# Performance work log

Measured on AMD Instinct MI355X. Metric: run time of the kernel, lower is better.

## Reference

```python
import jax, jax.numpy as jnp
import numpy as np

E = 2048   # embedding_size
H = 16     # n_heads
D = E // H # head_dimension = 128
B = 4
N = 2048


def setup_inputs() -> dict:
    key = jax.random.key(0)
    ks = jax.random.split(key, 5)
    scale_qkv = 1.0 / np.sqrt(E)
    scale_fc = 1.0 / np.sqrt(E)
    return {
        "x": jax.random.normal(ks[0], (B, N, E), dtype=jnp.float32),
        # torch Linear(E, E + 2*D); stored as [in, out] for x @ W
        "w_qkv": jax.random.uniform(ks[1], (E, E + 2 * D), jnp.float32, -scale_qkv, scale_qkv),
        "b_qkv": jax.random.uniform(ks[2], (E + 2 * D,), jnp.float32, -scale_qkv, scale_qkv),
        "w_fc": jax.random.uniform(ks[3], (E, E), jnp.float32, -scale_fc, scale_fc),
        "b_fc": jax.random.uniform(ks[4], (E,), jnp.float32, -scale_fc, scale_fc),
    }


def reference(x, w_qkv, b_qkv, w_fc, b_fc):
    b, n, _ = x.shape
    qkv = x @ w_qkv + b_qkv                         # [B,N,E+2D]
    q = qkv[..., :E].reshape(b, n, H, D)            # [B,N,H,D]
    k = qkv[..., E:E + D]                           # [B,N,D] single KV head (MQA)
    v = qkv[..., E + D:]                            # [B,N,D]
    # scores: queries per head against shared keys
    scores = jnp.einsum("bnhd,bmd->bhnm", q, k) / jnp.sqrt(jnp.float32(D))
    # causal mask: triu(ones, diagonal=1) positions filled with -inf
    causal = jnp.triu(jnp.ones((n, n), dtype=bool), k=1)
    scores = jnp.where(causal, -jnp.inf, scores)
    attn = jax.nn.softmax(scores, axis=-1)          # [B,H,N,N]
    out = jnp.einsum("bhnm,bmd->bnhd", attn, v)     # [B,N,H,D]
    out = out.reshape(b, n, E)
    return out @ w_fc + b_fc                        # dropout=0 (eval): identity
```

## Files before the change

kernel.cpp:

```cpp
#include <hip/hip_runtime.h>

#define E_DIM 2048
#define H_NUM 16
#define D_HEAD 128
#define B_SZ 4
#define N_SEQ 2048
#define QKV_LD 2304
#define MROWS_T (B_SZ * N_SEQ)
#define PLS 40
#define SC2F 0.12751744802582937f

typedef __attribute__((ext_vector_type(8))) __bf16 bfx8;
typedef __attribute__((ext_vector_type(8))) short sx8;
typedef __attribute__((ext_vector_type(4))) short sx4;
typedef __attribute__((ext_vector_type(4))) float fx4;

__device__ __forceinline__ fx4 mfma_bf16(bfx8 a, bfx8 b, fx4 c) {
    return __builtin_amdgcn_mfma_f32_16x16x32_bf16(a, b, c, 0, 0, 0);
}

__device__ __forceinline__ short f2bf(float f) {
    unsigned u = __builtin_bit_cast(unsigned, f);
    u += 0x7FFFu + ((u >> 16) & 1u);
    return (short)(u >> 16);
}

__device__ __forceinline__ void gld_lds16(const void* g, void* l) {
    __builtin_amdgcn_global_load_lds((__attribute__((address_space(1))) void*)(void*)g,
                                     (__attribute__((address_space(3))) void*)l, 16, 0, 0);
}

__global__ __launch_bounds__(256) void cast_f32_bf16(const float* __restrict__ in,
                                                     short* __restrict__ out, int n) {
    int i = (blockIdx.x * 256 + threadIdx.x) * 4;
    if (i >= n) return;
    float4 v = *(const float4*)(in + i);
    sx4 r = {f2bf(v.x), f2bf(v.y), f2bf(v.z), f2bf(v.w)};
    *(sx4*)(out + i) = r;
}

__global__ __launch_bounds__(256) void transpose_cast(const float* __restrict__ in,
                                                      short* __restrict__ out, int R, int C) {
    __shared__ float tile[32][33];
    int c0 = blockIdx.x * 32, r0 = blockIdx.y * 32;
    int tx = threadIdx.x;
    for (int i = threadIdx.y; i < 32; i += 8)
        tile[i][tx] = in[(size_t)(r0 + i) * C + c0 + tx];
    __syncthreads();
    for (int i = threadIdx.y; i < 32; i += 8)
        out[(size_t)(c0 + i) * R + r0 + tx] = f2bf(tile[tx][i]);
}

__global__ __launch_bounds__(256) void v_transpose(const short* __restrict__ qkv,
                                                   short* __restrict__ vtg) {
    __shared__ short tile[32][33];
    int r0 = blockIdx.x * 32;
    int d0 = blockIdx.y * 32;
    int tx = threadIdx.x;
    for (int i = threadIdx.y; i < 32; i += 8)
        tile[i][tx] = qkv[(size_t)(r0 + i) * QKV_LD + (E_DIM + D_HEAD) + d0 + tx];
    __syncthreads();
    for (int i = threadIdx.y; i < 32; i += 8)
        vtg[(size_t)(d0 + i) * MROWS_T + r0 + tx] = tile[tx][i];
}

template <bool OUT_BF16, bool SCALE_Q>
__global__ __launch_bounds__(256) void gemm_bt(const short* __restrict__ A,
                                               const short* __restrict__ Bt,
                                               const float* __restrict__ bias,
                                               void* __restrict__ Cp,
                                               int M, int N, int K) {
    __shared__ __align__(16) short As[128 * 32];
    __shared__ __align__(16) short Bs[128 * 32];
    const int tid = threadIdx.x, wave = tid >> 6, lane = tid & 63;
    const int quad = lane >> 4, l16 = lane & 15;
    const int m0 = blockIdx.y * 128, n0 = blockIdx.x * 128;
    const int wm = (wave >> 1) * 64, wn = (wave & 1) * 64;
    const int srow = lane >> 2, scol = (lane & 3) * 8;

    fx4 acc[4][4];
#pragma unroll
    for (int mt = 0; mt < 4; ++mt)
#pragma unroll
        for (int nt = 0; nt < 4; ++nt) acc[mt][nt] = (fx4){0.f, 0.f, 0.f, 0.f};

    const short* Ag = A + (size_t)m0 * K;
    const short* Bg = Bt + (size_t)n0 * K;

    for (int k0 = 0; k0 < K; k0 += 32) {
#pragma unroll
        for (int i = 0; i < 2; ++i) {
            int chunk = wave * 2 + i;
            int row = chunk * 16 + srow;
            gld_lds16(Ag + (size_t)row * K + k0 + scol, &As[chunk * 512]);
            gld_lds16(Bg + (size_t)row * K + k0 + scol, &Bs[chunk * 512]);
        }
        __syncthreads();
        bfx8 af[4], bfr[4];
#pragma unroll
        for (int t = 0; t < 4; ++t) {
            af[t]  = *(const bfx8*)&As[(wm + t * 16 + l16) * 32 + quad * 8];
            bfr[t] = *(const bfx8*)&Bs[(wn + t * 16 + l16) * 32 + quad * 8];
        }
#pragma unroll
        for (int mt = 0; mt < 4; ++mt)
#pragma unroll
            for (int nt = 0; nt < 4; ++nt)
                acc[mt][nt] = mfma_bf16(af[mt], bfr[nt], acc[mt][nt]);
        __syncthreads();
    }

    const float scl = (SCALE_Q && n0 < E_DIM) ? SC2F : 1.0f;
    float bv[4];
#pragma unroll
    for (int nt = 0; nt < 4; ++nt) bv[nt] = bias[n0 + wn + nt * 16 + l16];

#pragma unroll
    for (int mt = 0; mt < 4; ++mt)
#pragma unroll
        for (int nt = 0; nt < 4; ++nt)
#pragma unroll
            for (int j = 0; j < 4; ++j) {
                int row = m0 + wm + mt * 16 + quad * 4 + j;
                int col = n0 + wn + nt * 16 + l16;
                float v = (acc[mt][nt][j] + bv[nt]) * scl;
                if (OUT_BF16)
                    ((short*)Cp)[(size_t)row * N + col] = f2bf(v);
                else
                    ((float*)Cp)[(size_t)row * N + col] = v;
            }
}

__global__ __launch_bounds__(256, 4) void attn_kernel(const short* __restrict__ qkv,
                                                      const short* __restrict__ vtg,
                                                      short* __restrict__ outp) {
    __shared__ __align__(16) short Ks[2][4096];
    __shared__ __align__(16) short Vt[2][4096];
    __shared__ __align__(16) short pl[4 * 16 * PLS];
    const int b = blockIdx.y >> 4, h = blockIdx.y & 15;
    const int tid = threadIdx.x, wave = tid >> 6, lane = tid & 63;
    const int quad = lane >> 4, l16 = lane & 15;
    const int srow = lane >> 2, sq = lane & 3;
    const size_t baseRow = (size_t)b * N_SEQ;
    short* plw = pl + wave * 16 * PLS;

    auto stage = [&](int k0, int bufi) {
#pragma unroll
        for (int i = 0; i < 2; ++i) {
            const int c = wave * 2 + i;
            gld_lds16(qkv + (baseRow + k0 + (c & 1) * 16 + srow) * QKV_LD + E_DIM +
                          (c >> 1) * 32 + sq * 8,
                      &Ks[bufi][c * 512]);
            gld_lds16(vtg + (size_t)(c * 16 + srow) * MROWS_T + baseRow + k0 + sq * 8,
                      &Vt[bufi][c * 512]);
        }
    };

#pragma unroll 1
    for (int half = 0; half < 2; ++half) {
        const int chunk = half ? (31 - blockIdx.x) : blockIdx.x;
        const int q0 = chunk * 64;
        const int rowb = q0 + wave * 16 + quad * 4;

        bfx8 aq[4];
        {
            const short* qb =
                qkv + (baseRow + q0 + wave * 16 + l16) * QKV_LD + h * D_HEAD + quad * 8;
#pragma unroll
            for (int c = 0; c < 4; ++c) aq[c] = *(const bfx8*)(qb + c * 32);
        }

        fx4 accO[8];
        float l_loc[4];
#pragma unroll
        for (int dt = 0; dt < 8; ++dt) accO[dt] = (fx4){0.f, 0.f, 0.f, 0.f};
#pragma unroll
        for (int j = 0; j < 4; ++j) l_loc[j] = 0.f;

        const int nbulk = 2 * chunk;
        const int nkt = nbulk + 2;

        __syncthreads();
        stage(0, 0);

#pragma unroll 1
        for (int kt = 0; kt < nkt; ++kt) {
            __syncthreads();
            if (kt + 1 < nkt) stage((kt + 1) << 5, (kt + 1) & 1);
            const short* ks = Ks[kt & 1];
            const short* vs = Vt[kt & 1];
            const int k0 = kt << 5;

            fx4 s0 = {0.f, 0.f, 0.f, 0.f}, s1 = {0.f, 0.f, 0.f, 0.f};
#pragma unroll
            for (int dc = 0; dc < 4; ++dc) {
                bfx8 kf0 = *(const bfx8*)&ks[(dc * 2 + 0) * 512 + l16 * 32 + quad * 8];
                bfx8 kf1 = *(const bfx8*)&ks[(dc * 2 + 1) * 512 + l16 * 32 + quad * 8];
                s0 = mfma_bf16(aq[dc], kf0, s0);
                s1 = mfma_bf16(aq[dc], kf1, s1);
            }

            const bool diag = kt >= nbulk;
            float p0a[4], p1a[4];
#pragma unroll
            for (int j = 0; j < 4; ++j) {
                float e0 = __builtin_amdgcn_exp2f(s0[j]);
                float e1 = __builtin_amdgcn_exp2f(s1[j]);
                if (diag) {
                    e0 = (k0 + l16 <= rowb + j) ? e0 : 0.f;
                    e1 = (k0 + 16 + l16 <= rowb + j) ? e1 : 0.f;
                }
                p0a[j] = e0;
                p1a[j] = e1;
                l_loc[j] += e0 + e1;
            }

#pragma unroll
            for (int j = 0; j < 4; ++j) {
                plw[(quad * 4 + j) * PLS + l16] = f2bf(p0a[j]);
                plw[(quad * 4 + j) * PLS + 16 + l16] = f2bf(p1a[j]);
            }
            sx8 aps = *(const sx8*)&plw[l16 * PLS + quad * 8];
            bfx8 ap = __builtin_bit_cast(bfx8, aps);
#pragma unroll
            for (int dt = 0; dt < 8; ++dt) {
                bfx8 bv = *(const bfx8*)&vs[dt * 512 + l16 * 32 + quad * 8];
                accO[dt] = mfma_bf16(ap, bv, accO[dt]);
            }
        }

#pragma unroll
        for (int off = 1; off < 16; off <<= 1)
#pragma unroll
            for (int j = 0; j < 4; ++j) l_loc[j] += __shfl_xor(l_loc[j], off);
#pragma unroll
        for (int j = 0; j < 4; ++j) {
            float rl = 1.0f / l_loc[j];
            size_t obase = (baseRow + rowb + j) * (size_t)E_DIM + h * D_HEAD + l16;
#pragma unroll
            for (int dt = 0; dt < 8; ++dt)
                outp[obase + dt * 16] = f2bf(accO[dt][j] * rl);
        }
    }
}

extern "C" void kernel_launch(void* const* d_in, const int* in_sizes, int n_in,
                              void* d_out, int out_size, void* d_ws, size_t ws_size,
                              hipStream_t stream) {
    const float* x     = (const float*)d_in[0];
    const float* w_qkv = (const float*)d_in[1];
    const float* b_qkv = (const float*)d_in[2];
    const float* w_fc  = (const float*)d_in[3];
    const float* b_fc  = (const float*)d_in[4];
    float* out = (float*)d_out;

    const size_t MROWS = (size_t)B_SZ * N_SEQ;
    short* xb    = (short*)d_ws;
    short* wqkvt = xb + MROWS * E_DIM;
    short* wfct  = wqkvt + (size_t)QKV_LD * E_DIM;
    short* qkvb  = wfct + (size_t)E_DIM * E_DIM;
    short* attnb = qkvb + MROWS * QKV_LD;
    short* vtg   = xb;

    cast_f32_bf16<<<dim3((int)(MROWS * E_DIM / 1024)), dim3(256), 0, stream>>>(
        x, xb, (int)(MROWS * E_DIM));
    transpose_cast<<<dim3(QKV_LD / 32, E_DIM / 32), dim3(32, 8), 0, stream>>>(
        w_qkv, wqkvt, E_DIM, QKV_LD);
    transpose_cast<<<dim3(E_DIM / 32, E_DIM / 32), dim3(32, 8), 0, stream>>>(
        w_fc, wfct, E_DIM, E_DIM);

    gemm_bt<true, true><<<dim3(QKV_LD / 128, (int)(MROWS / 128)), dim3(256), 0, stream>>>(
        xb, wqkvt, b_qkv, qkvb, (int)MROWS, QKV_LD, E_DIM);

    v_transpose<<<dim3(MROWS_T / 32, D_HEAD / 32), dim3(32, 8), 0, stream>>>(qkvb, vtg);

    attn_kernel<<<dim3(16, B_SZ * H_NUM), dim3(256), 0, stream>>>(qkvb, vtg, attnb);

    gemm_bt<false, false><<<dim3(E_DIM / 128, (int)(MROWS / 128)), dim3(256), 0, stream>>>(
        attnb, wfct, b_fc, out, (int)MROWS, E_DIM, E_DIM);
}
```

Baseline: 489.5 us.

## Double attention rows per wave, pack P writes, and remap GEMM blocks per XCD

Each attention wave now handles 32 query rows instead of 16, so every K and V fragment read from LDS is reused across two MFMA row tiles. The grid is halved and launch bounds drop to 2 blocks per SM to fit the extra registers. P is packed with v_cvt_pk_bf16_f32 into an interleaved key order, and V^T is permuted to match. MFMA sections get s_setprio, and both GEMMs remap workgroup IDs so consecutive tiles share an XCD for L2 locality. The cost is higher register pressure, lower occupancy and fewer blocks for the causal load balance.

Result: faster. 466.1 us (-4.8%).

```diff
diff --git a/kernel.cpp b/kernel.cpp
--- a/kernel.cpp
+++ b/kernel.cpp
@@ -13,6 +13,7 @@
 typedef __attribute__((ext_vector_type(8))) __bf16 bfx8;
 typedef __attribute__((ext_vector_type(8))) short sx8;
 typedef __attribute__((ext_vector_type(4))) short sx4;
+typedef __attribute__((ext_vector_type(2))) short sx2;
 typedef __attribute__((ext_vector_type(4))) float fx4;
 
 __device__ __forceinline__ fx4 mfma_bf16(bfx8 a, bfx8 b, fx4 c) {
@@ -23,6 +24,12 @@
     unsigned u = __builtin_bit_cast(unsigned, f);
     u += 0x7FFFu + ((u >> 16) & 1u);
     return (short)(u >> 16);
+}
+
+__device__ __forceinline__ int cvt_pk_bf16(float a, float b) {
+    int r;
+    asm("v_cvt_pk_bf16_f32 %0, %1, %2" : "=v"(r) : "v"(a), "v"(b));
+    return r;
 }
 
 __device__ __forceinline__ void gld_lds16(const void* g, void* l) {
@@ -60,8 +67,9 @@
     for (int i = threadIdx.y; i < 32; i += 8)
         tile[i][tx] = qkv[(size_t)(r0 + i) * QKV_LD + (E_DIM + D_HEAD) + d0 + tx];
     __syncthreads();
+    int kp = ((tx & 15) << 1) | (tx >> 4);
     for (int i = threadIdx.y; i < 32; i += 8)
-        vtg[(size_t)(d0 + i) * MROWS_T + r0 + tx] = tile[tx][i];
+        vtg[(size_t)(d0 + i) * MROWS_T + r0 + kp] = tile[tx][i];
 }
 
 template <bool OUT_BF16, bool SCALE_Q>
@@ -74,7 +82,17 @@
     __shared__ __align__(16) short Bs[128 * 32];
     const int tid = threadIdx.x, wave = tid >> 6, lane = tid & 63;
     const int quad = lane >> 4, l16 = lane & 15;
-    const int m0 = blockIdx.y * 128, n0 = blockIdx.x * 128;
+
+    const int gx = gridDim.x;
+    int wg = blockIdx.y * gx + blockIdx.x;
+    {
+        const int nwg = gx * gridDim.y;
+        const int qd = nwg >> 3, rm = nwg & 7;
+        const int xcd = wg & 7, loc = wg >> 3;
+        wg = (xcd < rm ? xcd * (qd + 1) : rm * (qd + 1) + (xcd - rm) * qd) + loc;
+    }
+    const int m0 = (wg / gx) * 128, n0 = (wg % gx) * 128;
+
     const int wm = (wave >> 1) * 64, wn = (wave & 1) * 64;
     const int srow = lane >> 2, scol = (lane & 3) * 8;
 
@@ -131,18 +149,18 @@
             }
 }
 
-__global__ __launch_bounds__(256, 4) void attn_kernel(const short* __restrict__ qkv,
+__global__ __launch_bounds__(256, 2) void attn_kernel(const short* __restrict__ qkv,
                                                       const short* __restrict__ vtg,
                                                       short* __restrict__ outp) {
     __shared__ __align__(16) short Ks[2][4096];
     __shared__ __align__(16) short Vt[2][4096];
-    __shared__ __align__(16) short pl[4 * 16 * PLS];
+    __shared__ __align__(16) short pl[4 * 32 * PLS];
     const int b = blockIdx.y >> 4, h = blockIdx.y & 15;
     const int tid = threadIdx.x, wave = tid >> 6, lane = tid & 63;
     const int quad = lane >> 4, l16 = lane & 15;
     const int srow = lane >> 2, sq = lane & 3;
     const size_t baseRow = (size_t)b * N_SEQ;
-    short* plw = pl + wave * 16 * PLS;
+    short* plw = pl + wave * 32 * PLS;
 
     auto stage = [&](int k0, int bufi) {
 #pragma unroll
@@ -158,27 +176,33 @@
 
 #pragma unroll 1
     for (int half = 0; half < 2; ++half) {
-        const int chunk = half ? (31 - blockIdx.x) : blockIdx.x;
-        const int q0 = chunk * 64;
-        const int rowb = q0 + wave * 16 + quad * 4;
-
-        bfx8 aq[4];
+        const int chunk = half ? (15 - blockIdx.x) : blockIdx.x;
+        const int q0 = chunk * 128;
+        const int wrow = q0 + wave * 32;
+
+        bfx8 aq0[4], aq1[4];
         {
-            const short* qb =
-                qkv + (baseRow + q0 + wave * 16 + l16) * QKV_LD + h * D_HEAD + quad * 8;
-#pragma unroll
-            for (int c = 0; c < 4; ++c) aq[c] = *(const bfx8*)(qb + c * 32);
-        }
-
-        fx4 accO[8];
-        float l_loc[4];
-#pragma unroll
-        for (int dt = 0; dt < 8; ++dt) accO[dt] = (fx4){0.f, 0.f, 0.f, 0.f};
-#pragma unroll
-        for (int j = 0; j < 4; ++j) l_loc[j] = 0.f;
-
-        const int nbulk = 2 * chunk;
-        const int nkt = nbulk + 2;
+            const short* qb0 = qkv + (baseRow + wrow + l16) * QKV_LD + h * D_HEAD + quad * 8;
+            const short* qb1 = qb0 + 16 * QKV_LD;
+#pragma unroll
+            for (int c = 0; c < 4; ++c) {
+                aq0[c] = *(const bfx8*)(qb0 + c * 32);
+                aq1[c] = *(const bfx8*)(qb1 + c * 32);
+            }
+        }
+
+        fx4 accO0[8], accO1[8];
+        float l0[4], l1[4];
+#pragma unroll
+        for (int dt = 0; dt < 8; ++dt) {
+            accO0[dt] = (fx4){0.f, 0.f, 0.f, 0.f};
+            accO1[dt] = (fx4){0.f, 0.f, 0.f, 0.f};
+        }
+#pragma unroll
+        for (int j = 0; j < 4; ++j) { l0[j] = 0.f; l1[j] = 0.f; }
+
+        const int nbulk = 4 * chunk;
+        const int nkt = nbulk + 4;
 
         __syncthreads();
         stage(0, 0);
@@ -191,55 +215,80 @@
             const short* vs = Vt[kt & 1];
             const int k0 = kt << 5;
 
-            fx4 s0 = {0.f, 0.f, 0.f, 0.f}, s1 = {0.f, 0.f, 0.f, 0.f};
+            fx4 s00 = {0.f, 0.f, 0.f, 0.f}, s01 = {0.f, 0.f, 0.f, 0.f};
+            fx4 s10 = {0.f, 0.f, 0.f, 0.f}, s11 = {0.f, 0.f, 0.f, 0.f};
+            __builtin_amdgcn_s_setprio(1);
 #pragma unroll
             for (int dc = 0; dc < 4; ++dc) {
                 bfx8 kf0 = *(const bfx8*)&ks[(dc * 2 + 0) * 512 + l16 * 32 + quad * 8];
                 bfx8 kf1 = *(const bfx8*)&ks[(dc * 2 + 1) * 512 + l16 * 32 + quad * 8];
-                s0 = mfma_bf16(aq[dc], kf0, s0);
-                s1 = mfma_bf16(aq[dc], kf1, s1);
-            }
+                s00 = mfma_bf16(aq0[dc], kf0, s00);
+                s01 = mfma_bf16(aq0[dc], kf1, s01);
+                s10 = mfma_bf16(aq1[dc], kf0, s10);
+                s11 = mfma_bf16(aq1[dc], kf1, s11);
+            }
+            __builtin_amdgcn_s_setprio(0);
 
             const bool diag = kt >= nbulk;
-            float p0a[4], p1a[4];
 #pragma unroll
             for (int j = 0; j < 4; ++j) {
-                float e0 = __builtin_amdgcn_exp2f(s0[j]);
-                float e1 = __builtin_amdgcn_exp2f(s1[j]);
+                float e0 = __builtin_amdgcn_exp2f(s00[j]);
+                float e1 = __builtin_amdgcn_exp2f(s01[j]);
                 if (diag) {
-                    e0 = (k0 + l16 <= rowb + j) ? e0 : 0.f;
-                    e1 = (k0 + 16 + l16 <= rowb + j) ? e1 : 0.f;
+                    const int rb = wrow + quad * 4 + j;
+                    e0 = (k0 + l16 <= rb) ? e0 : 0.f;
+                    e1 = (k0 + 16 + l16 <= rb) ? e1 : 0.f;
                 }
-                p0a[j] = e0;
-                p1a[j] = e1;
-                l_loc[j] += e0 + e1;
-            }
-
+                l0[j] += e0 + e1;
+                int pk = cvt_pk_bf16(e0, e1);
+                *(sx2*)&plw[(quad * 4 + j) * PLS + 2 * l16] = __builtin_bit_cast(sx2, pk);
+            }
 #pragma unroll
             for (int j = 0; j < 4; ++j) {
-                plw[(quad * 4 + j) * PLS + l16] = f2bf(p0a[j]);
-                plw[(quad * 4 + j) * PLS + 16 + l16] = f2bf(p1a[j]);
-            }
-            sx8 aps = *(const sx8*)&plw[l16 * PLS + quad * 8];
-            bfx8 ap = __builtin_bit_cast(bfx8, aps);
+                float e0 = __builtin_amdgcn_exp2f(s10[j]);
+                float e1 = __builtin_amdgcn_exp2f(s11[j]);
+                if (diag) {
+                    const int rb = wrow + 16 + quad * 4 + j;
+                    e0 = (k0 + l16 <= rb) ? e0 : 0.f;
+                    e1 = (k0 + 16 + l16 <= rb) ? e1 : 0.f;
+                }
+                l1[j] += e0 + e1;
+                int pk = cvt_pk_bf16(e0, e1);
+                *(sx2*)&plw[(16 + quad * 4 + j) * PLS + 2 * l16] = __builtin_bit_cast(sx2, pk);
+            }
+
+            sx8 aps0 = *(const sx8*)&plw[l16 * PLS + quad * 8];
+            sx8 aps1 = *(const sx8*)&plw[(16 + l16) * PLS + quad * 8];
+            bfx8 ap0 = __builtin_bit_cast(bfx8, aps0);
+            bfx8 ap1 = __builtin_bit_cast(bfx8, aps1);
+            __builtin_amdgcn_s_setprio(1);
 #pragma unroll
             for (int dt = 0; dt < 8; ++dt) {
                 bfx8 bv = *(const bfx8*)&vs[dt * 512 + l16 * 32 + quad * 8];
-                accO[dt] = mfma_bf16(ap, bv, accO[dt]);
-            }
+                accO0[dt] = mfma_bf16(ap0, bv, accO0[dt]);
+                accO1[dt] = mfma_bf16(ap1, bv, accO1[dt]);
+            }
+            __builtin_amdgcn_s_setprio(0);
         }
 
 #pragma unroll
         for (int off = 1; off < 16; off <<= 1)
 #pragma unroll
-            for (int j = 0; j < 4; ++j) l_loc[j] += __shfl_xor(l_loc[j], off);
+            for (int j = 0; j < 4; ++j) {
+                l0[j] += __shfl_xor(l0[j], off);
+                l1[j] += __shfl_xor(l1[j], off);
+            }
 #pragma unroll
         for (int j = 0; j < 4; ++j) {
-            float rl = 1.0f / l_loc[j];
-            size_t obase = (baseRow + rowb + j) * (size_t)E_DIM + h * D_HEAD + l16;
-#pragma unroll
-            for (int dt = 0; dt < 8; ++dt)
-                outp[obase + dt * 16] = f2bf(accO[dt][j] * rl);
+            float rl0 = 1.0f / l0[j];
+            float rl1 = 1.0f / l1[j];
+            size_t ob0 = (baseRow + wrow + quad * 4 + j) * (size_t)E_DIM + h * D_HEAD + l16;
+            size_t ob1 = ob0 + (size_t)16 * E_DIM;
+#pragma unroll
+            for (int dt = 0; dt < 8; ++dt) {
+                outp[ob0 + dt * 16] = f2bf(accO0[dt][j] * rl0);
+                outp[ob1 + dt * 16] = f2bf(accO1[dt][j] * rl1);
+            }
         }
     }
 }
@@ -274,7 +323,7 @@
 
     v_transpose<<<dim3(MROWS_T / 32, D_HEAD / 32), dim3(32, 8), 0, stream>>>(qkvb, vtg);
 
-    attn_kernel<<<dim3(16, B_SZ * H_NUM), dim3(256), 0, stream>>>(qkvb, vtg, attnb);
+    attn_kernel<<<dim3(8, B_SZ * H_NUM), dim3(256), 0, stream>>>(qkvb, vtg, attnb);
 
     gemm_bt<false, false><<<dim3(E_DIM / 128, (int)(MROWS / 128)), dim3(256), 0, stream>>>(
         attnb, wfct, b_fc, out, (int)MROWS, E_DIM, E_DIM);
```
